# Kernel tuning notes

Hardware: AMD Instinct MI355X
Metric: run time of the kernel (lower is better)

## Reference

```python
import math
import jax, jax.numpy as jnp
import numpy as np

GRID = 16          # img_size // patch_size = 224 // 14
N_PER_H = 2048     # n_neurons // n_head = 8192 // 4
THETA = 10000.0


def _freqs_2d():
    """2D RoPE phase table, shape (1, 1, GRID*GRID, N_PER_H).
    Layout per position: [h_phases | w_phases | h_phases | w_phases], each half_dim//2 wide.
    """
    dim = N_PER_H
    half = dim // 2
    inv_freq = 1.0 / THETA ** (jnp.arange(0, half, 2, dtype=jnp.float32) / half)  # (half//2,)
    pos = jnp.arange(GRID, dtype=jnp.float32)
    ph = pos[:, None] * inv_freq[None, :]                       # (GRID, half//2)
    ph_h = jnp.broadcast_to(ph[:, None, :], (GRID, GRID, half // 2))
    ph_w = jnp.broadcast_to(ph[None, :, :], (GRID, GRID, half // 2))
    phases = jnp.concatenate([ph_h, ph_w, ph_h, ph_w], axis=-1)  # (GRID, GRID, dim)
    return phases.reshape(1, 1, GRID * GRID, dim)


def _rope(phases, v):
    ang = (phases % 1.0) * (2.0 * math.pi)
    c = jnp.cos(ang)
    s = jnp.sin(ang)
    # interleaved rotation: (-v_odd, v_even) re-interleaved
    v_rot = jnp.stack((-v[..., 1::2], v[..., ::2]), axis=-1).reshape(v.shape)
    return (v * c).astype(v.dtype) + (v_rot * s).astype(v.dtype)


def setup_inputs() -> dict:
    key = jax.random.key(0)
    kq, kk, kv = jax.random.split(key, 3)
    B, H, T, N = 16, 4, 256, N_PER_H
    D = 256
    Q = jax.random.normal(kq, (B, H, T, N), dtype=jnp.float32)
    K = jax.random.normal(kk, (B, H, T, N), dtype=jnp.float32)
    V = jax.random.normal(kv, (B, 1, T, D), dtype=jnp.float32)
    return {"Q": Q, "K": K, "V": V}


def reference(Q, K, V):
    B, H, T, N = Q.shape
    n_patches = GRID * GRID
    freqs = _freqs_2d()[:, :, :n_patches, :N]
    if T == n_patches + 1:  # static-shape branch (CLS token)
        Qr = jnp.concatenate([Q[:, :, :1, :], _rope(freqs, Q[:, :, 1:, :])], axis=2)
        Kr = jnp.concatenate([K[:, :, :1, :], _rope(freqs, K[:, :, 1:, :])], axis=2)
    else:
        f = freqs[:, :, :T, :]
        Qr = _rope(f, Q)
        Kr = _rope(f, K)
    # non-softmax bidirectional attention
    scores = jnp.einsum('bhtn,bhsn->bhts', Qr, Kr) / math.sqrt(N)  # (B,H,T,T)
    return jnp.matmul(scores, V)  # V (B,1,T,D) broadcasts over H -> (B,H,T,D)
```

## Files before the change

kernel.cpp:

```cpp
#include <hip/hip_runtime.h>
#include <hip/hip_bf16.h>

#define T_  256
#define NN_ 2048

typedef short bf16x8 __attribute__((ext_vector_type(8)));
typedef float f32x4  __attribute__((ext_vector_type(4)));

__device__ __forceinline__ unsigned short f2bf(float x) {
    union { float f; unsigned u; } v; v.f = x;
    unsigned r = v.u + 0x7fffu + ((v.u >> 16) & 1u);
    return (unsigned short)(r >> 16);
}
__device__ __forceinline__ float bflo(unsigned w) {
    union { unsigned u; float f; } v; v.u = w << 16; return v.f;
}
__device__ __forceinline__ float bfhi(unsigned w) {
    union { unsigned u; float f; } v; v.u = w & 0xffff0000u; return v.f;
}
__device__ __forceinline__ unsigned pkbf(float lo, float hi) {
    union { __hip_bfloat16 h; unsigned short s; } a, b;
    a.h = __float2bfloat16(lo);
    b.h = __float2bfloat16(hi);
    return (unsigned)a.s | ((unsigned)b.s << 16);
}

__device__ __forceinline__ void gld_lds16(const unsigned short* g, unsigned short* l) {
    __builtin_amdgcn_global_load_lds(
        (const __attribute__((address_space(1))) unsigned int*)g,
        (__attribute__((address_space(3))) unsigned int*)l, 16, 0, 0);
}

__global__ void build_cs(unsigned* __restrict__ cs) {
    int idx = blockIdx.x * 256 + threadIdx.x;
    int p = idx >> 9, f = idx & 511;
    float inv = powf(10000.0f, -(float)f * (1.0f / 512.0f));
    float ph  = (float)p * inv;
    float ang = (ph - floorf(ph)) * 6.28318530717958647692f;
    float s, c;
    sincosf(ang, &s, &c);
    cs[idx] = pkbf(c, s);
}

__global__ void vtrans(const float* __restrict__ V, unsigned short* __restrict__ Vt) {
    __shared__ unsigned short Tl[64 * 72];
    const int tid = threadIdx.x;
    const int b  = blockIdx.x >> 4;
    const int s0 = ((blockIdx.x >> 2) & 3) << 6;
    const int d0 = (blockIdx.x & 3) << 6;
    const float* Vb = V + (size_t)b * 65536;
#pragma unroll
    for (int u = 0; u < 4; u++) {
        int lin = u * 256 + tid;
        int srow = lin >> 4, c4 = (lin & 15) << 2;
        float4 v = *(const float4*)(Vb + (size_t)(s0 + srow) * 256 + d0 + c4);
        Tl[(c4 + 0) * 72 + srow] = f2bf(v.x);
        Tl[(c4 + 1) * 72 + srow] = f2bf(v.y);
        Tl[(c4 + 2) * 72 + srow] = f2bf(v.z);
        Tl[(c4 + 3) * 72 + srow] = f2bf(v.w);
    }
    __syncthreads();
    unsigned short* Vtb = Vt + (size_t)b * 65536;
#pragma unroll
    for (int u = 0; u < 2; u++) {
        int lin = u * 256 + tid;
        int drow = lin >> 3, sc8 = (lin & 7) << 3;
        *(uint4*)(Vtb + (size_t)(d0 + drow) * 256 + s0 + sc8) =
            *(const uint4*)(&Tl[drow * 72 + sc8]);
    }
}

__device__ __forceinline__ uint4 rot8(float4 q0, float4 q1,
                                      const uint4& c0, const uint4& c1, float sc) {
    q0.x *= sc; q0.y *= sc; q0.z *= sc; q0.w *= sc;
    q1.x *= sc; q1.y *= sc; q1.z *= sc; q1.w *= sc;
    uint4 o;
    o.x = pkbf(q0.x * bflo(c0.x) - q0.y * bfhi(c0.x),
               q0.y * bflo(c0.y) + q0.x * bfhi(c0.y));
    o.y = pkbf(q0.z * bflo(c0.z) - q0.w * bfhi(c0.z),
               q0.w * bflo(c0.w) + q0.z * bfhi(c0.w));
    o.z = pkbf(q1.x * bflo(c1.x) - q1.y * bfhi(c1.x),
               q1.y * bflo(c1.y) + q1.x * bfhi(c1.y));
    o.w = pkbf(q1.z * bflo(c1.z) - q1.w * bfhi(c1.z),
               q1.w * bflo(c1.w) + q1.z * bfhi(c1.w));
    return o;
}

#define RSC 0.02209708691207961f

__launch_bounds__(256, 3)
__global__ void rope_cast(const float* __restrict__ Q, const float* __restrict__ K,
                          const unsigned* __restrict__ cs,
                          unsigned short* __restrict__ Qr, unsigned short* __restrict__ Kr) {
    const int tid = threadIdx.x;
    const int bh  = blockIdx.x >> 4;
    const int hi  = blockIdx.x & 15;
    const size_t base = ((size_t)bh << 19) + ((size_t)hi << 15) + (size_t)tid * 8;
    const float* Qb = Q + base;
    const float* Kb = K + base;
    unsigned short* Qo = Qr + base;
    unsigned short* Ko = Kr + base;
    const int w = (tid >> 6) & 1;
    const int f = (tid * 8) & 511;

    if (w == 0) {
        const unsigned* cp = cs + (hi << 9) + f;
        const uint4 c0 = *(const uint4*)cp;
        const uint4 c1 = *(const uint4*)(cp + 4);
        float4 aq0 = *(const float4*)(Qb);
        float4 aq1 = *(const float4*)(Qb + 4);
        float4 ak0 = *(const float4*)(Kb);
        float4 ak1 = *(const float4*)(Kb + 4);
#pragma unroll
        for (int r2 = 0; r2 < 8; r2++) {
            const int e = r2 * 2;
            float4 bq0 = *(const float4*)(Qb + (e + 1) * 2048);
            float4 bq1 = *(const float4*)(Qb + (e + 1) * 2048 + 4);
            float4 bk0 = *(const float4*)(Kb + (e + 1) * 2048);
            float4 bk1 = *(const float4*)(Kb + (e + 1) * 2048 + 4);
            *(uint4*)(Qo + e * 2048) = rot8(aq0, aq1, c0, c1, RSC);
            *(uint4*)(Ko + e * 2048) = rot8(ak0, ak1, c0, c1, 1.0f);
            if (e + 2 < 16) {
                aq0 = *(const float4*)(Qb + (e + 2) * 2048);
                aq1 = *(const float4*)(Qb + (e + 2) * 2048 + 4);
                ak0 = *(const float4*)(Kb + (e + 2) * 2048);
                ak1 = *(const float4*)(Kb + (e + 2) * 2048 + 4);
            }
            *(uint4*)(Qo + (e + 1) * 2048) = rot8(bq0, bq1, c0, c1, RSC);
            *(uint4*)(Ko + (e + 1) * 2048) = rot8(bk0, bk1, c0, c1, 1.0f);
        }
    } else {
        const unsigned* cpb = cs + f;
        uint4 ca0 = *(const uint4*)(cpb);
        uint4 ca1 = *(const uint4*)(cpb + 4);
        float4 aq0 = *(const float4*)(Qb);
        float4 aq1 = *(const float4*)(Qb + 4);
        float4 ak0 = *(const float4*)(Kb);
        float4 ak1 = *(const float4*)(Kb + 4);
#pragma unroll
        for (int r2 = 0; r2 < 8; r2++) {
            const int e = r2 * 2;
            uint4 cb0 = *(const uint4*)(cpb + ((e + 1) << 9));
            uint4 cb1 = *(const uint4*)(cpb + ((e + 1) << 9) + 4);
            float4 bq0 = *(const float4*)(Qb + (e + 1) * 2048);
            float4 bq1 = *(const float4*)(Qb + (e + 1) * 2048 + 4);
            float4 bk0 = *(const float4*)(Kb + (e + 1) * 2048);
            float4 bk1 = *(const float4*)(Kb + (e + 1) * 2048 + 4);
            *(uint4*)(Qo + e * 2048) = rot8(aq0, aq1, ca0, ca1, RSC);
            *(uint4*)(Ko + e * 2048) = rot8(ak0, ak1, ca0, ca1, 1.0f);
            if (e + 2 < 16) {
                ca0 = *(const uint4*)(cpb + ((e + 2) << 9));
                ca1 = *(const uint4*)(cpb + ((e + 2) << 9) + 4);
                aq0 = *(const float4*)(Qb + (e + 2) * 2048);
                aq1 = *(const float4*)(Qb + (e + 2) * 2048 + 4);
                ak0 = *(const float4*)(Kb + (e + 2) * 2048);
                ak1 = *(const float4*)(Kb + (e + 2) * 2048 + 4);
            }
            *(uint4*)(Qo + (e + 1) * 2048) = rot8(bq0, bq1, cb0, cb1, RSC);
            *(uint4*)(Ko + (e + 1) * 2048) = rot8(bk0, bk1, cb0, cb1, 1.0f);
        }
    }
}

__launch_bounds__(256)
__global__ void gemm1b(const unsigned short* __restrict__ Qr,
                       const unsigned short* __restrict__ Kr,
                       unsigned short* __restrict__ scores) {
    __shared__ __align__(16) unsigned short A[128 * 64];
    __shared__ __align__(16) unsigned short Bt[64 * 64];

    const int tid  = threadIdx.x;
    const int bh   = blockIdx.x & 63;
    const int tile = blockIdx.x >> 6;
    const int ti = (tile >> 2) << 7;
    const int si = (tile & 3) << 6;

    const unsigned short* Qb = Qr + (size_t)bh * (T_ * NN_);
    const unsigned short* Kb = Kr + (size_t)bh * (T_ * NN_);

    const unsigned short* srcA[4]; unsigned short* dstA[4];
    const unsigned short* srcB[2]; unsigned short* dstB[2];
#pragma unroll
    for (int u = 0; u < 4; u++) {
        int lin = u * 256 + tid;
        int row = lin >> 3, cu = lin & 7;
        int scol = cu ^ (row & 7);
        srcA[u] = Qb + (size_t)(ti + row) * NN_ + scol * 8;
        dstA[u] = &A[lin * 8];
    }
#pragma unroll
    for (int u = 0; u < 2; u++) {
        int lin = u * 256 + tid;
        int row = lin >> 3, cu = lin & 7;
        int scol = cu ^ (row & 7);
        srcB[u] = Kb + (size_t)(si + row) * NN_ + scol * 8;
        dstB[u] = &Bt[lin * 8];
    }

    const int wv = tid >> 6, lane = tid & 63;
    const int lr = lane & 15, lg = lane >> 4;
    const int m0 = (wv >> 1) * 64;
    const int n0 = (wv & 1) * 32;

    f32x4 acc[4][2];
#pragma unroll
    for (int i = 0; i < 4; i++)
#pragma unroll
        for (int j = 0; j < 2; j++) acc[i][j] = (f32x4){0.f, 0.f, 0.f, 0.f};

    for (int k0 = 0; k0 < NN_; k0 += 64) {
#pragma unroll
        for (int u = 0; u < 4; u++) gld_lds16(srcA[u] + k0, dstA[u]);
#pragma unroll
        for (int u = 0; u < 2; u++) gld_lds16(srcB[u] + k0, dstB[u]);
        __syncthreads();

#pragma unroll
        for (int kk = 0; kk < 64; kk += 32) {
            bf16x8 af[4], bfr[2];
#pragma unroll
            for (int mi = 0; mi < 4; mi++) {
                int row = m0 + mi * 16 + lr;
                int c   = (kk >> 3) + lg;
                af[mi] = *(const bf16x8*)(&A[row * 64 + ((c ^ (row & 7)) << 3)]);
            }
#pragma unroll
            for (int ni = 0; ni < 2; ni++) {
                int row = n0 + ni * 16 + lr;
                int c   = (kk >> 3) + lg;
                bfr[ni] = *(const bf16x8*)(&Bt[row * 64 + ((c ^ (row & 7)) << 3)]);
            }
#pragma unroll
            for (int mi = 0; mi < 4; mi++)
#pragma unroll
                for (int ni = 0; ni < 2; ni++)
                    acc[mi][ni] = __builtin_amdgcn_mfma_f32_16x16x32_bf16(
                        af[mi], bfr[ni], acc[mi][ni], 0, 0, 0);
        }
        __syncthreads();
    }

    unsigned short* sb = scores + (size_t)bh * (T_ * T_);
#pragma unroll
    for (int mi = 0; mi < 4; mi++) {
        int tr = ti + m0 + mi * 16 + lg * 4;
#pragma unroll
        for (int ni = 0; ni < 2; ni++) {
            int sc = si + n0 + ni * 16 + lr;
#pragma unroll
            for (int r = 0; r < 4; r++)
                sb[(size_t)(tr + r) * 256 + sc] = f2bf(acc[mi][ni][r]);
        }
    }
}

__launch_bounds__(256)
__global__ void gemm2b(const unsigned short* __restrict__ scores,
                       const unsigned short* __restrict__ Vt, float* __restrict__ out) {
    __shared__ __align__(16) unsigned short A[128 * 64];
    __shared__ __align__(16) unsigned short Bt[64 * 64];

    const int tid  = threadIdx.x;
    const int bh   = blockIdx.x & 63;
    const int b    = bh >> 2;
    const int tile = blockIdx.x >> 6;
    const int ti = (tile >> 2) << 7;
    const int d0 = (tile & 3) << 6;

    const unsigned short* Sb  = scores + (size_t)bh * 65536;
    const unsigned short* Vtb = Vt + (size_t)b * 65536;

    const unsigned short* srcA[4]; unsigned short* dstA[4];
    const unsigned short* srcB[2]; unsigned short* dstB[2];
#pragma unroll
    for (int u = 0; u < 4; u++) {
        int lin = u * 256 + tid;
        int row = lin >> 3, cu = lin & 7;
        int scol = cu ^ (row & 7);
        srcA[u] = Sb + (size_t)(ti + row) * 256 + scol * 8;
        dstA[u] = &A[lin * 8];
    }
#pragma unroll
    for (int u = 0; u < 2; u++) {
        int lin = u * 256 + tid;
        int row = lin >> 3, cu = lin & 7;
        int scol = cu ^ (row & 7);
        srcB[u] = Vtb + (size_t)(d0 + row) * 256 + scol * 8;
        dstB[u] = &Bt[lin * 8];
    }

    const int wv = tid >> 6, lane = tid & 63;
    const int lr = lane & 15, lg = lane >> 4;
    const int m0 = (wv >> 1) * 64;
    const int n0 = (wv & 1) * 32;

    f32x4 acc[4][2];
#pragma unroll
    for (int i = 0; i < 4; i++)
#pragma unroll
        for (int j = 0; j < 2; j++) acc[i][j] = (f32x4){0.f, 0.f, 0.f, 0.f};

    for (int k0 = 0; k0 < 256; k0 += 64) {
#pragma unroll
        for (int u = 0; u < 4; u++) gld_lds16(srcA[u] + k0, dstA[u]);
#pragma unroll
        for (int u = 0; u < 2; u++) gld_lds16(srcB[u] + k0, dstB[u]);
        __syncthreads();

#pragma unroll
        for (int kk = 0; kk < 64; kk += 32) {
            bf16x8 af[4], bfr[2];
#pragma unroll
            for (int mi = 0; mi < 4; mi++) {
                int row = m0 + mi * 16 + lr;
                int c   = (kk >> 3) + lg;
                af[mi] = *(const bf16x8*)(&A[row * 64 + ((c ^ (row & 7)) << 3)]);
            }
#pragma unroll
            for (int ni = 0; ni < 2; ni++) {
                int row = n0 + ni * 16 + lr;
                int c   = (kk >> 3) + lg;
                bfr[ni] = *(const bf16x8*)(&Bt[row * 64 + ((c ^ (row & 7)) << 3)]);
            }
#pragma unroll
            for (int mi = 0; mi < 4; mi++)
#pragma unroll
                for (int ni = 0; ni < 2; ni++)
                    acc[mi][ni] = __builtin_amdgcn_mfma_f32_16x16x32_bf16(
                        af[mi], bfr[ni], acc[mi][ni], 0, 0, 0);
        }
        __syncthreads();
    }

    float* ob = out + (size_t)bh * 65536;
#pragma unroll
    for (int mi = 0; mi < 4; mi++) {
        int tr = ti + m0 + mi * 16 + lg * 4;
#pragma unroll
        for (int ni = 0; ni < 2; ni++) {
            int dc = d0 + n0 + ni * 16 + lr;
#pragma unroll
            for (int r = 0; r < 4; r++)
                ob[(size_t)(tr + r) * 256 + dc] = acc[mi][ni][r];
        }
    }
}

extern "C" void kernel_launch(void* const* d_in, const int* in_sizes, int n_in,
                              void* d_out, int out_size, void* d_ws, size_t ws_size,
                              hipStream_t stream) {
    const float* Q = (const float*)d_in[0];
    const float* K = (const float*)d_in[1];
    const float* V = (const float*)d_in[2];
    float* out = (float*)d_out;

    unsigned* cs = (unsigned*)d_ws;
    unsigned short* scores = (unsigned short*)((char*)d_ws + 32768);
    unsigned short* Vt = (unsigned short*)((char*)d_ws + 32768 + 8388608);
    unsigned short* Qr = (unsigned short*)((char*)d_ws + 16777216);
    unsigned short* Kr = (unsigned short*)((char*)d_ws + 83886080);

    build_cs<<<dim3(32), dim3(256), 0, stream>>>(cs);
    vtrans<<<dim3(256), dim3(256), 0, stream>>>(V, Vt);
    rope_cast<<<dim3(1024), dim3(256), 0, stream>>>(Q, K, cs, Qr, Kr);
    gemm1b<<<dim3(512), dim3(256), 0, stream>>>(Qr, Kr, scores);
    gemm2b<<<dim3(512), dim3(256), 0, stream>>>(scores, Vt, out);
}
```

Measured before the change: 147.7 us.

## Flatten rope_cast into grid-strided float4 elementwise kernel with computed cos/sin offsets

Rewrites the RoPE+bf16 cast kernel as a flat elementwise pass: each thread handles 8 float4 chunks of Q and K spread across the tensor, computes the cos/sin table offset per chunk, and issues all loads before a sched barrier and the stores. The grid grows from 1024 to 4096 blocks and the occupancy hint is dropped. This aims to improve memory-level parallelism and coalescing for a bandwidth-bound pass, at the cost of more table lookups per element and smaller 8-byte stores.

```diff
diff --git a/kernel.cpp b/kernel.cpp
--- a/kernel.cpp
+++ b/kernel.cpp
@@ -70,95 +70,58 @@
     }
 }
 
-__device__ __forceinline__ uint4 rot8(float4 q0, float4 q1,
-                                      const uint4& c0, const uint4& c1, float sc) {
-    q0.x *= sc; q0.y *= sc; q0.z *= sc; q0.w *= sc;
-    q1.x *= sc; q1.y *= sc; q1.z *= sc; q1.w *= sc;
-    uint4 o;
-    o.x = pkbf(q0.x * bflo(c0.x) - q0.y * bfhi(c0.x),
-               q0.y * bflo(c0.y) + q0.x * bfhi(c0.y));
-    o.y = pkbf(q0.z * bflo(c0.z) - q0.w * bfhi(c0.z),
-               q0.w * bflo(c0.w) + q0.z * bfhi(c0.w));
-    o.z = pkbf(q1.x * bflo(c1.x) - q1.y * bfhi(c1.x),
-               q1.y * bflo(c1.y) + q1.x * bfhi(c1.y));
-    o.w = pkbf(q1.z * bflo(c1.z) - q1.w * bfhi(c1.z),
-               q1.w * bflo(c1.w) + q1.z * bfhi(c1.w));
+#define RSC 0.02209708691207961f
+
+__device__ __forceinline__ uint2 rot4(float4 q, const uint4& c, float sc) {
+    q.x *= sc; q.y *= sc; q.z *= sc; q.w *= sc;
+    uint2 o;
+    o.x = pkbf(q.x * bflo(c.x) - q.y * bfhi(c.x),
+               q.y * bflo(c.y) + q.x * bfhi(c.y));
+    o.y = pkbf(q.z * bflo(c.z) - q.w * bfhi(c.z),
+               q.w * bflo(c.w) + q.z * bfhi(c.w));
     return o;
 }
 
-#define RSC 0.02209708691207961f
-
-__launch_bounds__(256, 3)
+__device__ __forceinline__ unsigned csoff(unsigned u) {
+    unsigned t = (u >> 9) & 255u;
+    unsigned p = ((u >> 7) & 1u) ? (t & 15u) : (t >> 4);
+    return (p << 9) + ((u & 127u) << 2);
+}
+
+__launch_bounds__(256)
 __global__ void rope_cast(const float* __restrict__ Q, const float* __restrict__ K,
                           const unsigned* __restrict__ cs,
                           unsigned short* __restrict__ Qr, unsigned short* __restrict__ Kr) {
-    const int tid = threadIdx.x;
-    const int bh  = blockIdx.x >> 4;
-    const int hi  = blockIdx.x & 15;
-    const size_t base = ((size_t)bh << 19) + ((size_t)hi << 15) + (size_t)tid * 8;
-    const float* Qb = Q + base;
-    const float* Kb = K + base;
-    unsigned short* Qo = Qr + base;
-    unsigned short* Ko = Kr + base;
-    const int w = (tid >> 6) & 1;
-    const int f = (tid * 8) & 511;
-
-    if (w == 0) {
-        const unsigned* cp = cs + (hi << 9) + f;
-        const uint4 c0 = *(const uint4*)cp;
-        const uint4 c1 = *(const uint4*)(cp + 4);
-        float4 aq0 = *(const float4*)(Qb);
-        float4 aq1 = *(const float4*)(Qb + 4);
-        float4 ak0 = *(const float4*)(Kb);
-        float4 ak1 = *(const float4*)(Kb + 4);
-#pragma unroll
-        for (int r2 = 0; r2 < 8; r2++) {
-            const int e = r2 * 2;
-            float4 bq0 = *(const float4*)(Qb + (e + 1) * 2048);
-            float4 bq1 = *(const float4*)(Qb + (e + 1) * 2048 + 4);
-            float4 bk0 = *(const float4*)(Kb + (e + 1) * 2048);
-            float4 bk1 = *(const float4*)(Kb + (e + 1) * 2048 + 4);
-            *(uint4*)(Qo + e * 2048) = rot8(aq0, aq1, c0, c1, RSC);
-            *(uint4*)(Ko + e * 2048) = rot8(ak0, ak1, c0, c1, 1.0f);
-            if (e + 2 < 16) {
-                aq0 = *(const float4*)(Qb + (e + 2) * 2048);
-                aq1 = *(const float4*)(Qb + (e + 2) * 2048 + 4);
-                ak0 = *(const float4*)(Kb + (e + 2) * 2048);
-                ak1 = *(const float4*)(Kb + (e + 2) * 2048 + 4);
-            }
-            *(uint4*)(Qo + (e + 1) * 2048) = rot8(bq0, bq1, c0, c1, RSC);
-            *(uint4*)(Ko + (e + 1) * 2048) = rot8(bk0, bk1, c0, c1, 1.0f);
-        }
-    } else {
-        const unsigned* cpb = cs + f;
-        uint4 ca0 = *(const uint4*)(cpb);
-        uint4 ca1 = *(const uint4*)(cpb + 4);
-        float4 aq0 = *(const float4*)(Qb);
-        float4 aq1 = *(const float4*)(Qb + 4);
-        float4 ak0 = *(const float4*)(Kb);
-        float4 ak1 = *(const float4*)(Kb + 4);
-#pragma unroll
-        for (int r2 = 0; r2 < 8; r2++) {
-            const int e = r2 * 2;
-            uint4 cb0 = *(const uint4*)(cpb + ((e + 1) << 9));
-            uint4 cb1 = *(const uint4*)(cpb + ((e + 1) << 9) + 4);
-            float4 bq0 = *(const float4*)(Qb + (e + 1) * 2048);
-            float4 bq1 = *(const float4*)(Qb + (e + 1) * 2048 + 4);
-            float4 bk0 = *(const float4*)(Kb + (e + 1) * 2048);
-            float4 bk1 = *(const float4*)(Kb + (e + 1) * 2048 + 4);
-            *(uint4*)(Qo + e * 2048) = rot8(aq0, aq1, ca0, ca1, RSC);
-            *(uint4*)(Ko + e * 2048) = rot8(ak0, ak1, ca0, ca1, 1.0f);
-            if (e + 2 < 16) {
-                ca0 = *(const uint4*)(cpb + ((e + 2) << 9));
-                ca1 = *(const uint4*)(cpb + ((e + 2) << 9) + 4);
-                aq0 = *(const float4*)(Qb + (e + 2) * 2048);
-                aq1 = *(const float4*)(Qb + (e + 2) * 2048 + 4);
-                ak0 = *(const float4*)(Kb + (e + 2) * 2048);
-                ak1 = *(const float4*)(Kb + (e + 2) * 2048 + 4);
-            }
-            *(uint4*)(Qo + (e + 1) * 2048) = rot8(bq0, bq1, cb0, cb1, RSC);
-            *(uint4*)(Ko + (e + 1) * 2048) = rot8(bk0, bk1, cb0, cb1, 1.0f);
-        }
+    const unsigned gid = blockIdx.x * 256 + threadIdx.x;
+#pragma unroll
+    for (int c = 0; c < 2; c++) {
+        const unsigned u0 = gid + (unsigned)(4 * c + 0) * 1048576u;
+        const unsigned u1 = gid + (unsigned)(4 * c + 1) * 1048576u;
+        const unsigned u2 = gid + (unsigned)(4 * c + 2) * 1048576u;
+        const unsigned u3 = gid + (unsigned)(4 * c + 3) * 1048576u;
+
+        float4 dq0 = *(const float4*)(Q + (size_t)u0 * 4);
+        float4 dq1 = *(const float4*)(Q + (size_t)u1 * 4);
+        float4 dq2 = *(const float4*)(Q + (size_t)u2 * 4);
+        float4 dq3 = *(const float4*)(Q + (size_t)u3 * 4);
+        float4 dk0 = *(const float4*)(K + (size_t)u0 * 4);
+        float4 dk1 = *(const float4*)(K + (size_t)u1 * 4);
+        float4 dk2 = *(const float4*)(K + (size_t)u2 * 4);
+        float4 dk3 = *(const float4*)(K + (size_t)u3 * 4);
+        uint4 cc0 = *(const uint4*)(cs + csoff(u0));
+        uint4 cc1 = *(const uint4*)(cs + csoff(u1));
+        uint4 cc2 = *(const uint4*)(cs + csoff(u2));
+        uint4 cc3 = *(const uint4*)(cs + csoff(u3));
+        __builtin_amdgcn_sched_barrier(0);
+
+        *(uint2*)(Qr + (size_t)u0 * 4) = rot4(dq0, cc0, RSC);
+        *(uint2*)(Kr + (size_t)u0 * 4) = rot4(dk0, cc0, 1.0f);
+        *(uint2*)(Qr + (size_t)u1 * 4) = rot4(dq1, cc1, RSC);
+        *(uint2*)(Kr + (size_t)u1 * 4) = rot4(dk1, cc1, 1.0f);
+        *(uint2*)(Qr + (size_t)u2 * 4) = rot4(dq2, cc2, RSC);
+        *(uint2*)(Kr + (size_t)u2 * 4) = rot4(dk2, cc2, 1.0f);
+        *(uint2*)(Qr + (size_t)u3 * 4) = rot4(dq3, cc3, RSC);
+        *(uint2*)(Kr + (size_t)u3 * 4) = rot4(dk3, cc3, 1.0f);
     }
 }
 
@@ -362,7 +325,7 @@
 
     build_cs<<<dim3(32), dim3(256), 0, stream>>>(cs);
     vtrans<<<dim3(256), dim3(256), 0, stream>>>(V, Vt);
-    rope_cast<<<dim3(1024), dim3(256), 0, stream>>>(Q, K, cs, Qr, Kr);
+    rope_cast<<<dim3(4096), dim3(256), 0, stream>>>(Q, K, cs, Qr, Kr);
     gemm1b<<<dim3(512), dim3(256), 0, stream>>>(Qr, Kr, scores);
     gemm2b<<<dim3(512), dim3(256), 0, stream>>>(scores, Vt, out);
 }
```

Result: no change. 149.3 us (+1.1%).
